# Optimization experiments

Measured on AMD Instinct MI355X. Metric: run time of the kernel, lower is better.

Reference implementation:

```python
import jax, jax.numpy as jnp
import numpy as np

EPS = 1e-5  # BatchNorm2d default eps; running stats at init: mean=0, var=1


def conv_bn_silu(x, w, gamma, beta):
    # 1x1 conv (no bias) + BatchNorm (mean=0, var=1) + SiLU
    y = jnp.einsum('bchw,oc->bohw', x, w)
    y = y * (gamma / jnp.sqrt(1.0 + EPS))[None, :, None, None] + beta[None, :, None, None]
    return jax.nn.silu(y)


def setup_inputs() -> dict:
    key = jax.random.key(0)
    ks = jax.random.split(key, 13)
    c1, c2 = 256, 256
    ci = c2 // 8   # 32  (theta/phi)
    cg = c2 // 2   # 128 (g)
    b, h, w = 8, 56, 56
    sd = lambda cin: 1.0 / np.sqrt(cin)
    return {
        'x':       jax.random.normal(ks[0], (b, c1, h, w), jnp.float32),
        'w_theta': jax.random.normal(ks[1], (ci, c1), jnp.float32) * sd(c1),
        'g_theta': jnp.ones((ci,), jnp.float32),
        'b_theta': jnp.zeros((ci,), jnp.float32),
        'w_phi':   jax.random.normal(ks[2], (ci, c1), jnp.float32) * sd(c1),
        'g_phi':   jnp.ones((ci,), jnp.float32),
        'b_phi':   jnp.zeros((ci,), jnp.float32),
        'w_g':     jax.random.normal(ks[3], (cg, c1), jnp.float32) * sd(c1),
        'g_g':     jnp.ones((cg,), jnp.float32),
        'b_g':     jnp.zeros((cg,), jnp.float32),
        'w_out':   jax.random.normal(ks[4], (c2, cg), jnp.float32) * sd(cg),
        'g_out':   jnp.ones((c2,), jnp.float32),
        'b_out':   jnp.zeros((c2,), jnp.float32),
    }


def reference(x, w_theta, g_theta, b_theta, w_phi, g_phi, b_phi,
              w_g, g_g, b_g, w_out, g_out, b_out):
    b, c, h, w = x.shape
    hw = h * w
    theta = conv_bn_silu(x, w_theta, g_theta, b_theta).reshape(b, -1, hw).transpose(0, 2, 1)  # [b,hw,ci]
    phi   = conv_bn_silu(x, w_phi,   g_phi,   b_phi).reshape(b, -1, hw)                       # [b,ci,hw]
    g     = conv_bn_silu(x, w_g,     g_g,     b_g).reshape(b, -1, hw).transpose(0, 2, 1)      # [b,hw,cg]
    attn = jax.nn.softmax(jnp.einsum('bnc,bcm->bnm', theta, phi), axis=-1)                    # [b,hw,hw]
    out = jnp.einsum('bnm,bmc->bnc', attn, g).transpose(0, 2, 1).reshape(b, -1, h, w)         # [b,cg,h,w]
    return conv_bn_silu(out, w_out, g_out, b_out) + x
```

## Files before the change

### kernel.cpp

```cpp
#include <hip/hip_runtime.h>

typedef __bf16 bf16;
typedef __bf16 bf16x4 __attribute__((ext_vector_type(4)));
typedef __bf16 bf16x8 __attribute__((ext_vector_type(8)));
typedef float f32x4 __attribute__((ext_vector_type(4)));

#define MFMA16(a,b,c) __builtin_amdgcn_mfma_f32_16x16x32_bf16((a),(b),(c),0,0,0)

__device__ __forceinline__ float silu_f(float y){ return y/(1.f+__expf(-y)); }

__device__ __forceinline__ bf16x8 ld8f(const float* __restrict__ p){
    float4 a = *(const float4*)p;
    float4 b = *(const float4*)(p+4);
    bf16x8 r;
    r[0]=(bf16)a.x; r[1]=(bf16)a.y; r[2]=(bf16)a.z; r[3]=(bf16)a.w;
    r[4]=(bf16)b.x; r[5]=(bf16)b.y; r[6]=(bf16)b.z; r[7]=(bf16)b.w;
    return r;
}

#define BN_SCALE 0.9999950000374997f

__global__ __launch_bounds__(256) void qkv_kernel(
    const float* __restrict__ xg,
    const float* __restrict__ wth, const float* __restrict__ gth, const float* __restrict__ bth,
    const float* __restrict__ wph, const float* __restrict__ gph, const float* __restrict__ bph,
    const float* __restrict__ wgg, const float* __restrict__ ggg, const float* __restrict__ bgg,
    bf16* __restrict__ Qb, bf16* __restrict__ Kb, bf16* __restrict__ Vtb)
{
    const int b = blockIdx.x, pt = blockIdx.y;
    const int p0 = pt*64;
    const int t = threadIdx.x;
    const int lane = t & 63, wv = t >> 6;
    const int lc = lane & 15, lg = lane >> 4;

    __shared__ __align__(16) bf16 xT[64][264];

    {
        const int cbase = t >> 4;
        const int p4 = (t & 15) * 4;
        #pragma unroll
        for (int r = 0; r < 16; ++r) {
            int c = r*16 + cbase;
            float4 v = *(const float4*)(xg + ((size_t)(b*256 + c))*3136 + p0 + p4);
            xT[p4+0][c] = (bf16)v.x; xT[p4+1][c] = (bf16)v.y;
            xT[p4+2][c] = (bf16)v.z; xT[p4+3][c] = (bf16)v.w;
        }
    }
    __syncthreads();

    const f32x4 fz = {0.f,0.f,0.f,0.f};

    for (int tt = 0; tt < 3; ++tt) {
        const int ot = wv*3 + tt;
        if (ot < 4) {
            const float *W, *gam, *bet; bf16* dst; int ol;
            if (ot < 2) { W=wth; gam=gth; bet=bth; dst=Qb; ol=ot*16; }
            else        { W=wph; gam=gph; bet=bph; dst=Kb; ol=(ot-2)*16; }
            f32x4 acc[4]; acc[0]=fz; acc[1]=fz; acc[2]=fz; acc[3]=fz;
            #pragma unroll
            for (int ks = 0; ks < 8; ++ks) {
                bf16x8 wf = ld8f(W + (size_t)(ol+lc)*256 + ks*32 + lg*8);
                #pragma unroll
                for (int pf = 0; pf < 4; ++pf) {
                    bf16x8 af = *(const bf16x8*)&xT[pf*16+lc][ks*32+lg*8];
                    acc[pf] = MFMA16(af, wf, acc[pf]);
                }
            }
            const int oc = ol + lc;
            const float sc = gam[oc] * BN_SCALE;
            const float bi = bet[oc];
            #pragma unroll
            for (int pf = 0; pf < 4; ++pf)
                #pragma unroll
                for (int r = 0; r < 4; ++r) {
                    int pos = p0 + pf*16 + lg*4 + r;
                    dst[((size_t)b*3136 + pos)*32 + oc] = (bf16)silu_f(acc[pf][r]*sc + bi);
                }
        } else {
            const int ol = (ot-4)*16;
            f32x4 acc[4]; acc[0]=fz; acc[1]=fz; acc[2]=fz; acc[3]=fz;
            #pragma unroll
            for (int ks = 0; ks < 8; ++ks) {
                bf16x8 wf = ld8f(wgg + (size_t)(ol+lc)*256 + ks*32 + lg*8);
                #pragma unroll
                for (int pc = 0; pc < 4; ++pc) {
                    bf16x8 xf = *(const bf16x8*)&xT[pc*16+lc][ks*32+lg*8];
                    acc[pc] = MFMA16(wf, xf, acc[pc]);
                }
            }
            #pragma unroll
            for (int r = 0; r < 4; ++r) {
                const int oc = ol + lg*4 + r;
                const float sc = ggg[oc] * BN_SCALE;
                const float bi = bgg[oc];
                #pragma unroll
                for (int pc = 0; pc < 4; ++pc) {
                    int pos = p0 + pc*16 + lc;
                    Vtb[((size_t)b*128 + oc)*3136 + pos] = (bf16)silu_f(acc[pc][r]*sc + bi);
                }
            }
        }
    }
}

__global__ __launch_bounds__(256) void attn_kernel(
    const bf16* __restrict__ Qb, const bf16* __restrict__ Kb,
    const bf16* __restrict__ Vtb, bf16* __restrict__ Opart,
    float* __restrict__ mpart, float* __restrict__ lpart)
{
    const int b = blockIdx.x, qt = blockIdx.y, z = blockIdx.z;
    const int kt0 = (z==0) ? 0  : 13 + 12*(z-1);
    const int kt1 = (z==3) ? 49 : 13 + 12*z;
    const int p0 = qt*64;
    const int t = threadIdx.x;
    const int lane = t & 63, wv = t >> 6;
    const int lc = lane & 15, lg = lane >> 4;

    __shared__ __align__(16) bf16 Klds[64][40];
    __shared__ __align__(16) bf16 Vlds[128*64];
    __shared__ __align__(16) bf16 Plds[4][16*72];

    const bf16* Kbase = Kb + (size_t)b*3136*32;
    const bf16* Vbase = Vtb + (size_t)b*128*3136;

    bf16x8 qf = *(const bf16x8*)(Qb + ((size_t)b*3136 + p0 + wv*16 + lc)*32 + lg*8);

    float mrow[4] = {-1e30f,-1e30f,-1e30f,-1e30f};
    float lrow[4] = {0.f,0.f,0.f,0.f};
    const f32x4 fz = {0.f,0.f,0.f,0.f};
    f32x4 oacc[8];
    #pragma unroll
    for (int cf = 0; cf < 8; ++cf) oacc[cf] = fz;

    const int krow = t >> 2, kkp = (t & 3) * 8;
    const int vrow0 = t >> 3;
    const int vj    = t & 7;
    const int pxorw = (lg >> 1) << 4;
    const int pxorr = (lc >> 3) << 4;

    bf16x8 kreg; bf16x8 vreg0, vreg1, vreg2, vreg3;
    {
        const int k0 = kt0*64;
        kreg  = *(const bf16x8*)(Kbase + (size_t)(k0+krow)*32 + kkp);
        vreg0 = *(const bf16x8*)(Vbase + (size_t)(0*32+vrow0)*3136 + k0 + vj*8);
        vreg1 = *(const bf16x8*)(Vbase + (size_t)(1*32+vrow0)*3136 + k0 + vj*8);
        vreg2 = *(const bf16x8*)(Vbase + (size_t)(2*32+vrow0)*3136 + k0 + vj*8);
        vreg3 = *(const bf16x8*)(Vbase + (size_t)(3*32+vrow0)*3136 + k0 + vj*8);
    }
    const int vxor = (vrow0 & 7) << 4;

    for (int kt = kt0; kt < kt1; ++kt) {
        __syncthreads();
        *(bf16x8*)&Klds[krow][kkp] = kreg;
        *(bf16x8*)((char*)Vlds + (0*32+vrow0)*128 + ((vj*16) ^ vxor)) = vreg0;
        *(bf16x8*)((char*)Vlds + (1*32+vrow0)*128 + ((vj*16) ^ vxor)) = vreg1;
        *(bf16x8*)((char*)Vlds + (2*32+vrow0)*128 + ((vj*16) ^ vxor)) = vreg2;
        *(bf16x8*)((char*)Vlds + (3*32+vrow0)*128 + ((vj*16) ^ vxor)) = vreg3;
        __syncthreads();

        if (kt+1 < kt1) {
            const int kn = (kt+1)*64;
            kreg  = *(const bf16x8*)(Kbase + (size_t)(kn+krow)*32 + kkp);
            vreg0 = *(const bf16x8*)(Vbase + (size_t)(0*32+vrow0)*3136 + kn + vj*8);
            vreg1 = *(const bf16x8*)(Vbase + (size_t)(1*32+vrow0)*3136 + kn + vj*8);
            vreg2 = *(const bf16x8*)(Vbase + (size_t)(2*32+vrow0)*3136 + kn + vj*8);
            vreg3 = *(const bf16x8*)(Vbase + (size_t)(3*32+vrow0)*3136 + kn + vj*8);
        }

        f32x4 s[4];
        #pragma unroll
        for (int nf = 0; nf < 4; ++nf) {
            bf16x8 kf = *(const bf16x8*)&Klds[nf*16+lc][lg*8];
            s[nf] = MFMA16(qf, kf, fz);
        }

        float mx[4];
        #pragma unroll
        for (int r = 0; r < 4; ++r) {
            float m = fmaxf(fmaxf(s[0][r], s[1][r]), fmaxf(s[2][r], s[3][r]));
            #pragma unroll
            for (int d = 1; d < 16; d <<= 1) m = fmaxf(m, __shfl_xor(m, d));
            mx[r] = m;
        }
        bool ok = (mx[0] <= mrow[0]+8.f) && (mx[1] <= mrow[1]+8.f)
               && (mx[2] <= mrow[2]+8.f) && (mx[3] <= mrow[3]+8.f);
        if (!__all(ok)) {
            float scale[4];
            #pragma unroll
            for (int r = 0; r < 4; ++r) {
                float nm = fmaxf(mrow[r], mx[r]);
                scale[r] = __expf(mrow[r] - nm);
                mrow[r] = nm;
                lrow[r] *= scale[r];
            }
            #pragma unroll
            for (int cf = 0; cf < 8; ++cf)
                #pragma unroll
                for (int r = 0; r < 4; ++r) oacc[cf][r] *= scale[r];
        }
        #pragma unroll
        for (int r = 0; r < 4; ++r) {
            float ps = 0.f;
            #pragma unroll
            for (int nf = 0; nf < 4; ++nf) {
                float pv = __expf(s[nf][r] - mrow[r]); s[nf][r] = pv; ps += pv;
            }
            #pragma unroll
            for (int d = 1; d < 16; d <<= 1) ps += __shfl_xor(ps, d);
            lrow[r] += ps;
        }

        #pragma unroll
        for (int nf = 0; nf < 4; ++nf)
            #pragma unroll
            for (int r = 0; r < 4; ++r)
                Plds[wv][(lg*4+r)*72 + ((nf*16+lc) ^ pxorw)] = (bf16)s[nf][r];

        __builtin_amdgcn_s_setprio(1);
        #pragma unroll
        for (int ks = 0; ks < 2; ++ks) {
            bf16x8 pfr = *(const bf16x8*)&Plds[wv][lc*72 + ((ks*32 + lg*8) ^ pxorr)];
            #pragma unroll
            for (int cf = 0; cf < 8; ++cf) {
                const int vrow = cf*16 + lc;
                bf16x8 vf = *(const bf16x8*)((char*)Vlds + vrow*128
                                 + ((ks*64 + lg*16) ^ ((vrow & 7) << 4)));
                oacc[cf] = MFMA16(pfr, vf, oacc[cf]);
            }
        }
        __builtin_amdgcn_s_setprio(0);
    }

    #pragma unroll
    for (int cf = 0; cf < 8; ++cf)
        #pragma unroll
        for (int r = 0; r < 4; ++r) {
            int q = p0 + wv*16 + lg*4 + r;
            Opart[((size_t)(z*8+b)*3136 + q)*128 + cf*16 + lc] = (bf16)oacc[cf][r];
        }
    if (lc == 0) {
        #pragma unroll
        for (int r = 0; r < 4; ++r) {
            int q = p0 + wv*16 + lg*4 + r;
            size_t idx = (size_t)(z*8+b)*3136 + q;
            mpart[idx] = mrow[r];
            lpart[idx] = lrow[r];
        }
    }
}

__global__ __launch_bounds__(256) void out_kernel(
    const bf16* __restrict__ Opart, const float* __restrict__ mpart,
    const float* __restrict__ lpart, const float* __restrict__ wout,
    const float* __restrict__ gout, const float* __restrict__ bout,
    const float* __restrict__ xg, float* __restrict__ outp)
{
    const int b = blockIdx.x, pt = blockIdx.y;
    const int p0 = pt*64;
    const int t = threadIdx.x;
    const int lane = t & 63, wv = t >> 6;
    const int lc = lane & 15, lg = lane >> 4;

    __shared__ __align__(16) bf16 Olds[64][136];
    __shared__ __align__(16) bf16 outlds[4][64][72];

    {
        const int row = t >> 2;
        const int cb = (t & 3) * 32;
        const int q = p0 + row;
        float m0 = mpart[(size_t)(0*8+b)*3136 + q];
        float m1 = mpart[(size_t)(1*8+b)*3136 + q];
        float m2 = mpart[(size_t)(2*8+b)*3136 + q];
        float m3 = mpart[(size_t)(3*8+b)*3136 + q];
        float M = fmaxf(fmaxf(m0,m1), fmaxf(m2,m3));
        float w0 = __expf(m0-M), w1 = __expf(m1-M), w2 = __expf(m2-M), w3 = __expf(m3-M);
        float L = lpart[(size_t)(0*8+b)*3136 + q]*w0 + lpart[(size_t)(1*8+b)*3136 + q]*w1
                + lpart[(size_t)(2*8+b)*3136 + q]*w2 + lpart[(size_t)(3*8+b)*3136 + q]*w3;
        float inv = 1.f / L;
        w0 *= inv; w1 *= inv; w2 *= inv; w3 *= inv;
        #pragma unroll
        for (int r = 0; r < 4; ++r) {
            int c8 = cb + r*8;
            float o[8];
            #pragma unroll
            for (int j = 0; j < 8; ++j) o[j] = 0.f;
            bf16x8 v0 = *(const bf16x8*)(Opart + ((size_t)(0*8+b)*3136 + q)*128 + c8);
            bf16x8 v1 = *(const bf16x8*)(Opart + ((size_t)(1*8+b)*3136 + q)*128 + c8);
            bf16x8 v2 = *(const bf16x8*)(Opart + ((size_t)(2*8+b)*3136 + q)*128 + c8);
            bf16x8 v3 = *(const bf16x8*)(Opart + ((size_t)(3*8+b)*3136 + q)*128 + c8);
            #pragma unroll
            for (int j = 0; j < 8; ++j)
                o[j] = w0*(float)v0[j] + w1*(float)v1[j] + w2*(float)v2[j] + w3*(float)v3[j];
            bf16x8 rr;
            #pragma unroll
            for (int j = 0; j < 8; ++j) rr[j] = (bf16)o[j];
            *(bf16x8*)&Olds[row][c8] = rr;
        }
    }
    __syncthreads();

    const f32x4 fz = {0.f,0.f,0.f,0.f};
    f32x4 acc[4][4];
    #pragma unroll
    for (int pf = 0; pf < 4; ++pf)
        #pragma unroll
        for (int nf = 0; nf < 4; ++nf) acc[pf][nf] = fz;

    #pragma unroll
    for (int ks = 0; ks < 4; ++ks) {
        bf16x8 wf[4];
        #pragma unroll
        for (int nf = 0; nf < 4; ++nf)
            wf[nf] = ld8f(wout + (size_t)(wv*64 + nf*16 + lc)*128 + ks*32 + lg*8);
        #pragma unroll
        for (int pf = 0; pf < 4; ++pf) {
            bf16x8 af = *(const bf16x8*)&Olds[pf*16+lc][ks*32+lg*8];
            #pragma unroll
            for (int nf = 0; nf < 4; ++nf)
                acc[pf][nf] = MFMA16(af, wf[nf], acc[pf][nf]);
        }
    }

    #pragma unroll
    for (int nf = 0; nf < 4; ++nf) {
        const int oc = wv*64 + nf*16 + lc;
        const float sc = gout[oc] * BN_SCALE;
        const float bi = bout[oc];
        #pragma unroll
        for (int pf = 0; pf < 4; ++pf)
            #pragma unroll
            for (int r = 0; r < 4; ++r)
                outlds[wv][nf*16+lc][pf*16+lg*4+r] = (bf16)silu_f(acc[pf][nf][r]*sc + bi);
    }

    #pragma unroll
    for (int i = 0; i < 16; ++i) {
        const int orow = i*4 + lg;
        const int oc = wv*64 + orow;
        const int p4 = lc*4;
        bf16x4 vo = *(const bf16x4*)&outlds[wv][orow][p4];
        float4 vx = *(const float4*)(xg + ((size_t)b*256 + oc)*3136 + p0 + p4);
        float4 res;
        res.x = (float)vo[0] + vx.x;
        res.y = (float)vo[1] + vx.y;
        res.z = (float)vo[2] + vx.z;
        res.w = (float)vo[3] + vx.w;
        *(float4*)(outp + ((size_t)b*256 + oc)*3136 + p0 + p4) = res;
    }
}

extern "C" void kernel_launch(void* const* d_in, const int* in_sizes, int n_in,
                              void* d_out, int out_size, void* d_ws, size_t ws_size,
                              hipStream_t stream)
{
    const float* x    = (const float*)d_in[0];
    const float* wth  = (const float*)d_in[1];
    const float* gth  = (const float*)d_in[2];
    const float* bth  = (const float*)d_in[3];
    const float* wph  = (const float*)d_in[4];
    const float* gph  = (const float*)d_in[5];
    const float* bph  = (const float*)d_in[6];
    const float* wgg  = (const float*)d_in[7];
    const float* ggg  = (const float*)d_in[8];
    const float* bgg  = (const float*)d_in[9];
    const float* wout = (const float*)d_in[10];
    const float* gout = (const float*)d_in[11];
    const float* bout = (const float*)d_in[12];

    bf16* ws  = (bf16*)d_ws;
    bf16* Qb    = ws;
    bf16* Kb    = Qb + (size_t)8*3136*32;
    bf16* Vtb   = Kb + (size_t)8*3136*32;
    bf16* Opart = Vtb + (size_t)8*128*3136;
    float* mpart = (float*)(Opart + (size_t)4*8*3136*128);
    float* lpart = mpart + (size_t)4*8*3136;

    dim3 blk(256);
    qkv_kernel<<<dim3(8,49), blk, 0, stream>>>(x, wth, gth, bth, wph, gph, bph,
                                               wgg, ggg, bgg, Qb, Kb, Vtb);
    attn_kernel<<<dim3(8,49,4), blk, 0, stream>>>(Qb, Kb, Vtb, Opart, mpart, lpart);
    out_kernel<<<dim3(8,49), blk, 0, stream>>>(Opart, mpart, lpart,
                                               wout, gout, bout, x, (float*)d_out);
}
```

Measured before the change: 221.8 us.

## Split attention KV into seven chunks, double-buffer LDS, use DPP reductions, halve conv tiles

The attention grid goes from 4 to 7 KV splits of 7 tiles each, so more blocks are in flight. K/V LDS tiles are double-buffered so one barrier per iteration is removed. Row max and sum reductions now use DPP row-rotate instead of shuffles. The qkv and output kernels use 32-position tiles with vectorised LDS transposes and stores, doubling their grid. In exchange the merge kernel reads more partial outputs, and LDS use in the attention kernel grows.

```diff
diff --git a/kernel.cpp b/kernel.cpp
--- a/kernel.cpp
+++ b/kernel.cpp
@@ -6,8 +6,28 @@
 typedef float f32x4 __attribute__((ext_vector_type(4)));
 
 #define MFMA16(a,b,c) __builtin_amdgcn_mfma_f32_16x16x32_bf16((a),(b),(c),0,0,0)
+#define NSPLIT 7
 
 __device__ __forceinline__ float silu_f(float y){ return y/(1.f+__expf(-y)); }
+
+template<int CTRL>
+__device__ __forceinline__ float ror_max(float x){
+    int y = __builtin_amdgcn_update_dpp(0, __builtin_bit_cast(int,x), CTRL, 0xf, 0xf, false);
+    return fmaxf(x, __builtin_bit_cast(float,y));
+}
+template<int CTRL>
+__device__ __forceinline__ float ror_add(float x){
+    int y = __builtin_amdgcn_update_dpp(0, __builtin_bit_cast(int,x), CTRL, 0xf, 0xf, false);
+    return x + __builtin_bit_cast(float,y);
+}
+__device__ __forceinline__ float red16_max(float x){
+    x = ror_max<0x128>(x); x = ror_max<0x124>(x);
+    x = ror_max<0x122>(x); x = ror_max<0x121>(x); return x;
+}
+__device__ __forceinline__ float red16_add(float x){
+    x = ror_add<0x128>(x); x = ror_add<0x124>(x);
+    x = ror_add<0x122>(x); x = ror_add<0x121>(x); return x;
+}
 
 __device__ __forceinline__ bf16x8 ld8f(const float* __restrict__ p){
     float4 a = *(const float4*)p;
@@ -28,22 +48,34 @@
     bf16* __restrict__ Qb, bf16* __restrict__ Kb, bf16* __restrict__ Vtb)
 {
     const int b = blockIdx.x, pt = blockIdx.y;
-    const int p0 = pt*64;
+    const int p0 = pt*32;
     const int t = threadIdx.x;
     const int lane = t & 63, wv = t >> 6;
     const int lc = lane & 15, lg = lane >> 4;
 
-    __shared__ __align__(16) bf16 xT[64][264];
+    __shared__ __align__(16) bf16 xT[32][264];
 
     {
-        const int cbase = t >> 4;
-        const int p4 = (t & 15) * 4;
-        #pragma unroll
-        for (int r = 0; r < 16; ++r) {
-            int c = r*16 + cbase;
-            float4 v = *(const float4*)(xg + ((size_t)(b*256 + c))*3136 + p0 + p4);
-            xT[p4+0][c] = (bf16)v.x; xT[p4+1][c] = (bf16)v.y;
-            xT[p4+2][c] = (bf16)v.z; xT[p4+3][c] = (bf16)v.w;
+        const int ci = t & 15;
+        const int pj = (t >> 4) & 7;
+        const int ch = t >> 7;
+        const int p4 = pj*4;
+        #pragma unroll
+        for (int r = 0; r < 2; ++r) {
+            const int c0 = (r*2 + ch)*64 + ci*4;
+            float va[4][4];
+            #pragma unroll
+            for (int k = 0; k < 4; ++k) {
+                float4 v = *(const float4*)(xg + ((size_t)(b*256 + c0 + k))*3136 + p0 + p4);
+                va[k][0]=v.x; va[k][1]=v.y; va[k][2]=v.z; va[k][3]=v.w;
+            }
+            #pragma unroll
+            for (int i = 0; i < 4; ++i) {
+                bf16x4 w;
+                w[0]=(bf16)va[0][i]; w[1]=(bf16)va[1][i];
+                w[2]=(bf16)va[2][i]; w[3]=(bf16)va[3][i];
+                *(bf16x4*)&xT[p4+i][c0] = w;
+            }
         }
     }
     __syncthreads();
@@ -56,12 +88,12 @@
             const float *W, *gam, *bet; bf16* dst; int ol;
             if (ot < 2) { W=wth; gam=gth; bet=bth; dst=Qb; ol=ot*16; }
             else        { W=wph; gam=gph; bet=bph; dst=Kb; ol=(ot-2)*16; }
-            f32x4 acc[4]; acc[0]=fz; acc[1]=fz; acc[2]=fz; acc[3]=fz;
+            f32x4 acc[2]; acc[0]=fz; acc[1]=fz;
             #pragma unroll
             for (int ks = 0; ks < 8; ++ks) {
                 bf16x8 wf = ld8f(W + (size_t)(ol+lc)*256 + ks*32 + lg*8);
                 #pragma unroll
-                for (int pf = 0; pf < 4; ++pf) {
+                for (int pf = 0; pf < 2; ++pf) {
                     bf16x8 af = *(const bf16x8*)&xT[pf*16+lc][ks*32+lg*8];
                     acc[pf] = MFMA16(af, wf, acc[pf]);
                 }
@@ -70,7 +102,7 @@
             const float sc = gam[oc] * BN_SCALE;
             const float bi = bet[oc];
             #pragma unroll
-            for (int pf = 0; pf < 4; ++pf)
+            for (int pf = 0; pf < 2; ++pf)
                 #pragma unroll
                 for (int r = 0; r < 4; ++r) {
                     int pos = p0 + pf*16 + lg*4 + r;
@@ -78,12 +110,12 @@
                 }
         } else {
             const int ol = (ot-4)*16;
-            f32x4 acc[4]; acc[0]=fz; acc[1]=fz; acc[2]=fz; acc[3]=fz;
+            f32x4 acc[2]; acc[0]=fz; acc[1]=fz;
             #pragma unroll
             for (int ks = 0; ks < 8; ++ks) {
                 bf16x8 wf = ld8f(wgg + (size_t)(ol+lc)*256 + ks*32 + lg*8);
                 #pragma unroll
-                for (int pc = 0; pc < 4; ++pc) {
+                for (int pc = 0; pc < 2; ++pc) {
                     bf16x8 xf = *(const bf16x8*)&xT[pc*16+lc][ks*32+lg*8];
                     acc[pc] = MFMA16(wf, xf, acc[pc]);
                 }
@@ -94,7 +126,7 @@
                 const float sc = ggg[oc] * BN_SCALE;
                 const float bi = bgg[oc];
                 #pragma unroll
-                for (int pc = 0; pc < 4; ++pc) {
+                for (int pc = 0; pc < 2; ++pc) {
                     int pos = p0 + pc*16 + lc;
                     Vtb[((size_t)b*128 + oc)*3136 + pos] = (bf16)silu_f(acc[pc][r]*sc + bi);
                 }
@@ -109,15 +141,14 @@
     float* __restrict__ mpart, float* __restrict__ lpart)
 {
     const int b = blockIdx.x, qt = blockIdx.y, z = blockIdx.z;
-    const int kt0 = (z==0) ? 0  : 13 + 12*(z-1);
-    const int kt1 = (z==3) ? 49 : 13 + 12*z;
+    const int kt0 = z*7, kt1 = kt0+7;
     const int p0 = qt*64;
     const int t = threadIdx.x;
     const int lane = t & 63, wv = t >> 6;
     const int lc = lane & 15, lg = lane >> 4;
 
-    __shared__ __align__(16) bf16 Klds[64][40];
-    __shared__ __align__(16) bf16 Vlds[128*64];
+    __shared__ __align__(16) bf16 Klds[2][64][40];
+    __shared__ __align__(16) bf16 Vlds[2][128*64];
     __shared__ __align__(16) bf16 Plds[4][16*72];
 
     const bf16* Kbase = Kb + (size_t)b*3136*32;
@@ -133,12 +164,12 @@
     for (int cf = 0; cf < 8; ++cf) oacc[cf] = fz;
 
     const int krow = t >> 2, kkp = (t & 3) * 8;
-    const int vrow0 = t >> 3;
-    const int vj    = t & 7;
+    const int vrow0 = t >> 3, vj = t & 7;
+    const int vxor = (vrow0 & 7) << 4;
     const int pxorw = (lg >> 1) << 4;
     const int pxorr = (lc >> 3) << 4;
 
-    bf16x8 kreg; bf16x8 vreg0, vreg1, vreg2, vreg3;
+    bf16x8 kreg, vreg0, vreg1, vreg2, vreg3;
     {
         const int k0 = kt0*64;
         kreg  = *(const bf16x8*)(Kbase + (size_t)(k0+krow)*32 + kkp);
@@ -147,15 +178,16 @@
         vreg2 = *(const bf16x8*)(Vbase + (size_t)(2*32+vrow0)*3136 + k0 + vj*8);
         vreg3 = *(const bf16x8*)(Vbase + (size_t)(3*32+vrow0)*3136 + k0 + vj*8);
     }
-    const int vxor = (vrow0 & 7) << 4;
-
+
+    int cur = 0;
     for (int kt = kt0; kt < kt1; ++kt) {
-        __syncthreads();
-        *(bf16x8*)&Klds[krow][kkp] = kreg;
-        *(bf16x8*)((char*)Vlds + (0*32+vrow0)*128 + ((vj*16) ^ vxor)) = vreg0;
-        *(bf16x8*)((char*)Vlds + (1*32+vrow0)*128 + ((vj*16) ^ vxor)) = vreg1;
-        *(bf16x8*)((char*)Vlds + (2*32+vrow0)*128 + ((vj*16) ^ vxor)) = vreg2;
-        *(bf16x8*)((char*)Vlds + (3*32+vrow0)*128 + ((vj*16) ^ vxor)) = vreg3;
+        bf16* Kl = &Klds[cur][0][0];
+        bf16* Vl = &Vlds[cur][0];
+        *(bf16x8*)&Kl[krow*40 + kkp] = kreg;
+        *(bf16x8*)((char*)Vl + (0*32+vrow0)*128 + ((vj*16) ^ vxor)) = vreg0;
+        *(bf16x8*)((char*)Vl + (1*32+vrow0)*128 + ((vj*16) ^ vxor)) = vreg1;
+        *(bf16x8*)((char*)Vl + (2*32+vrow0)*128 + ((vj*16) ^ vxor)) = vreg2;
+        *(bf16x8*)((char*)Vl + (3*32+vrow0)*128 + ((vj*16) ^ vxor)) = vreg3;
         __syncthreads();
 
         if (kt+1 < kt1) {
@@ -170,7 +202,7 @@
         f32x4 s[4];
         #pragma unroll
         for (int nf = 0; nf < 4; ++nf) {
-            bf16x8 kf = *(const bf16x8*)&Klds[nf*16+lc][lg*8];
+            bf16x8 kf = *(const bf16x8*)&Kl[(nf*16+lc)*40 + lg*8];
             s[nf] = MFMA16(qf, kf, fz);
         }
 
@@ -178,9 +210,7 @@
         #pragma unroll
         for (int r = 0; r < 4; ++r) {
             float m = fmaxf(fmaxf(s[0][r], s[1][r]), fmaxf(s[2][r], s[3][r]));
-            #pragma unroll
-            for (int d = 1; d < 16; d <<= 1) m = fmaxf(m, __shfl_xor(m, d));
-            mx[r] = m;
+            mx[r] = red16_max(m);
         }
         bool ok = (mx[0] <= mrow[0]+8.f) && (mx[1] <= mrow[1]+8.f)
                && (mx[2] <= mrow[2]+8.f) && (mx[3] <= mrow[3]+8.f);
@@ -205,9 +235,7 @@
             for (int nf = 0; nf < 4; ++nf) {
                 float pv = __expf(s[nf][r] - mrow[r]); s[nf][r] = pv; ps += pv;
             }
-            #pragma unroll
-            for (int d = 1; d < 16; d <<= 1) ps += __shfl_xor(ps, d);
-            lrow[r] += ps;
+            lrow[r] += red16_add(ps);
         }
 
         #pragma unroll
@@ -223,12 +251,13 @@
             #pragma unroll
             for (int cf = 0; cf < 8; ++cf) {
                 const int vrow = cf*16 + lc;
-                bf16x8 vf = *(const bf16x8*)((char*)Vlds + vrow*128
+                bf16x8 vf = *(const bf16x8*)((char*)Vl + vrow*128
                                  + ((ks*64 + lg*16) ^ ((vrow & 7) << 4)));
                 oacc[cf] = MFMA16(pfr, vf, oacc[cf]);
             }
         }
         __builtin_amdgcn_s_setprio(0);
+        cur ^= 1;
     }
 
     #pragma unroll
@@ -256,41 +285,46 @@
     const float* __restrict__ xg, float* __restrict__ outp)
 {
     const int b = blockIdx.x, pt = blockIdx.y;
-    const int p0 = pt*64;
+    const int p0 = pt*32;
     const int t = threadIdx.x;
     const int lane = t & 63, wv = t >> 6;
     const int lc = lane & 15, lg = lane >> 4;
 
-    __shared__ __align__(16) bf16 Olds[64][136];
-    __shared__ __align__(16) bf16 outlds[4][64][72];
+    __shared__ __align__(16) bf16 Olds[32][136];
+    __shared__ __align__(16) bf16 outlds[4][64][40];
 
     {
-        const int row = t >> 2;
-        const int cb = (t & 3) * 32;
+        const int row = t >> 3;
+        const int cc  = (t & 7) * 16;
         const int q = p0 + row;
-        float m0 = mpart[(size_t)(0*8+b)*3136 + q];
-        float m1 = mpart[(size_t)(1*8+b)*3136 + q];
-        float m2 = mpart[(size_t)(2*8+b)*3136 + q];
-        float m3 = mpart[(size_t)(3*8+b)*3136 + q];
-        float M = fmaxf(fmaxf(m0,m1), fmaxf(m2,m3));
-        float w0 = __expf(m0-M), w1 = __expf(m1-M), w2 = __expf(m2-M), w3 = __expf(m3-M);
-        float L = lpart[(size_t)(0*8+b)*3136 + q]*w0 + lpart[(size_t)(1*8+b)*3136 + q]*w1
-                + lpart[(size_t)(2*8+b)*3136 + q]*w2 + lpart[(size_t)(3*8+b)*3136 + q]*w3;
-        float inv = 1.f / L;
-        w0 *= inv; w1 *= inv; w2 *= inv; w3 *= inv;
-        #pragma unroll
-        for (int r = 0; r < 4; ++r) {
-            int c8 = cb + r*8;
+        float mz[NSPLIT], wz[NSPLIT];
+        float M = -1e30f;
+        #pragma unroll
+        for (int zz = 0; zz < NSPLIT; ++zz) {
+            mz[zz] = mpart[(size_t)(zz*8+b)*3136 + q];
+            M = fmaxf(M, mz[zz]);
+        }
+        float L = 0.f;
+        #pragma unroll
+        for (int zz = 0; zz < NSPLIT; ++zz) {
+            wz[zz] = __expf(mz[zz] - M);
+            L += lpart[(size_t)(zz*8+b)*3136 + q] * wz[zz];
+        }
+        const float inv = 1.f / L;
+        #pragma unroll
+        for (int zz = 0; zz < NSPLIT; ++zz) wz[zz] *= inv;
+        #pragma unroll
+        for (int h = 0; h < 2; ++h) {
+            const int c8 = cc + h*8;
             float o[8];
             #pragma unroll
             for (int j = 0; j < 8; ++j) o[j] = 0.f;
-            bf16x8 v0 = *(const bf16x8*)(Opart + ((size_t)(0*8+b)*3136 + q)*128 + c8);
-            bf16x8 v1 = *(const bf16x8*)(Opart + ((size_t)(1*8+b)*3136 + q)*128 + c8);
-            bf16x8 v2 = *(const bf16x8*)(Opart + ((size_t)(2*8+b)*3136 + q)*128 + c8);
-            bf16x8 v3 = *(const bf16x8*)(Opart + ((size_t)(3*8+b)*3136 + q)*128 + c8);
-            #pragma unroll
-            for (int j = 0; j < 8; ++j)
-                o[j] = w0*(float)v0[j] + w1*(float)v1[j] + w2*(float)v2[j] + w3*(float)v3[j];
+            #pragma unroll
+            for (int zz = 0; zz < NSPLIT; ++zz) {
+                bf16x8 v = *(const bf16x8*)(Opart + ((size_t)(zz*8+b)*3136 + q)*128 + c8);
+                #pragma unroll
+                for (int j = 0; j < 8; ++j) o[j] += wz[zz] * (float)v[j];
+            }
             bf16x8 rr;
             #pragma unroll
             for (int j = 0; j < 8; ++j) rr[j] = (bf16)o[j];
@@ -300,9 +334,9 @@
     __syncthreads();
 
     const f32x4 fz = {0.f,0.f,0.f,0.f};
-    f32x4 acc[4][4];
-    #pragma unroll
-    for (int pf = 0; pf < 4; ++pf)
+    f32x4 acc[2][4];
+    #pragma unroll
+    for (int pf = 0; pf < 2; ++pf)
         #pragma unroll
         for (int nf = 0; nf < 4; ++nf) acc[pf][nf] = fz;
 
@@ -313,7 +347,7 @@
         for (int nf = 0; nf < 4; ++nf)
             wf[nf] = ld8f(wout + (size_t)(wv*64 + nf*16 + lc)*128 + ks*32 + lg*8);
         #pragma unroll
-        for (int pf = 0; pf < 4; ++pf) {
+        for (int pf = 0; pf < 2; ++pf) {
             bf16x8 af = *(const bf16x8*)&Olds[pf*16+lc][ks*32+lg*8];
             #pragma unroll
             for (int nf = 0; nf < 4; ++nf)
@@ -327,17 +361,20 @@
         const float sc = gout[oc] * BN_SCALE;
         const float bi = bout[oc];
         #pragma unroll
-        for (int pf = 0; pf < 4; ++pf)
+        for (int pf = 0; pf < 2; ++pf) {
+            bf16x4 w;
             #pragma unroll
             for (int r = 0; r < 4; ++r)
-                outlds[wv][nf*16+lc][pf*16+lg*4+r] = (bf16)silu_f(acc[pf][nf][r]*sc + bi);
-    }
-
-    #pragma unroll
-    for (int i = 0; i < 16; ++i) {
-        const int orow = i*4 + lg;
+                w[r] = (bf16)silu_f(acc[pf][nf][r]*sc + bi);
+            *(bf16x4*)&outlds[wv][nf*16+lc][pf*16+lg*4] = w;
+        }
+    }
+
+    #pragma unroll
+    for (int i = 0; i < 8; ++i) {
+        const int orow = i*8 + (lane >> 3);
         const int oc = wv*64 + orow;
-        const int p4 = lc*4;
+        const int p4 = (lane & 7) * 4;
         bf16x4 vo = *(const bf16x4*)&outlds[wv][orow][p4];
         float4 vx = *(const float4*)(xg + ((size_t)b*256 + oc)*3136 + p0 + p4);
         float4 res;
@@ -372,13 +409,13 @@
     bf16* Kb    = Qb + (size_t)8*3136*32;
     bf16* Vtb   = Kb + (size_t)8*3136*32;
     bf16* Opart = Vtb + (size_t)8*128*3136;
-    float* mpart = (float*)(Opart + (size_t)4*8*3136*128);
-    float* lpart = mpart + (size_t)4*8*3136;
+    float* mpart = (float*)(Opart + (size_t)NSPLIT*8*3136*128);
+    float* lpart = mpart + (size_t)NSPLIT*8*3136;
 
     dim3 blk(256);
-    qkv_kernel<<<dim3(8,49), blk, 0, stream>>>(x, wth, gth, bth, wph, gph, bph,
+    qkv_kernel<<<dim3(8,98), blk, 0, stream>>>(x, wth, gth, bth, wph, gph, bph,
                                                wgg, ggg, bgg, Qb, Kb, Vtb);
-    attn_kernel<<<dim3(8,49,4), blk, 0, stream>>>(Qb, Kb, Vtb, Opart, mpart, lpart);
-    out_kernel<<<dim3(8,49), blk, 0, stream>>>(Opart, mpart, lpart,
+    attn_kernel<<<dim3(8,49,NSPLIT), blk, 0, stream>>>(Qb, Kb, Vtb, Opart, mpart, lpart);
+    out_kernel<<<dim3(8,98), blk, 0, stream>>>(Opart, mpart, lpart,
                                                wout, gout, bout, x, (float*)d_out);
 }
```

After: 214.8 us. -3.2%, faster.
